# Kernel tuning notes

Measured on AMD Instinct MI355X. Metric: run time of the kernel, lower is better.

Reference implementation:

```python
import jax, jax.numpy as jnp
import numpy as np

B, T, N, FIN, FOUT, EDIM = 2, 32, 64, 64, 64, 16
EPS = 1e-5

def _xavier(key, fan_in, fan_out):
    limit = np.sqrt(6.0 / (fan_in + fan_out))
    return jax.random.uniform(key, (fan_in, fan_out), minval=-limit, maxval=limit, dtype=jnp.float32)

def setup_inputs() -> dict:
    key = jax.random.key(0)
    ks = jax.random.split(key, 8)
    x = jax.random.normal(ks[0], (B, T, N, FIN), dtype=jnp.float32)
    adj = jax.random.uniform(ks[1], (B, N, N), dtype=jnp.float32)
    # edge_net: Linear(1->EDIM), GELU, Linear(EDIM->FIN*FOUT); stored as (in,out)
    ew1 = _xavier(ks[2], 1, EDIM)
    eb1 = jnp.zeros((EDIM,), jnp.float32)
    ew2 = _xavier(ks[3], EDIM, FIN * FOUT)
    eb2 = jnp.zeros((FIN * FOUT,), jnp.float32)
    # node_lin: Linear(FIN->FOUT)
    nw = _xavier(ks[4], FIN, FOUT)
    nb = jnp.zeros((FOUT,), jnp.float32)
    # GraphNorm params (pre_norm -> num_features = FIN)
    gw = jnp.ones((FIN,), jnp.float32)
    gb = jnp.zeros((FIN,), jnp.float32)
    gms = jnp.ones((1,), jnp.float32)
    return {"x": x, "adj": adj, "ew1": ew1, "eb1": eb1, "ew2": ew2, "eb2": eb2,
            "nw": nw, "nb": nb, "gw": gw, "gb": gb, "gms": gms}

def reference(x, adj, ew1, eb1, ew2, eb2, nw, nb, gw, gb, gms):
    # GraphNorm over node axis (dim=-2), pre-norm
    mean = jnp.mean(x, axis=-2, keepdims=True)
    var = jnp.var(x, axis=-2, keepdims=True)  # unbiased=False
    xn = (x - mean * gms) / jnp.sqrt(var + EPS)
    xn = xn * gw + gb  # (B,T,N,FIN)
    # edge-conditioned weights: scalar adj -> (B,N,N,FIN,FOUT)
    ef = adj[..., None]  # (B,N,N,1)
    h = jax.nn.gelu(ef @ ew1 + eb1, approximate=False)  # (B,N,N,EDIM)
    edge_w = (h @ ew2 + eb2).reshape(adj.shape[0], N, N, FIN, FOUT)
    # agg[b,t,i,o] = sum_j sum_f xn[b,t,j,f] * edge_w[b,i,j,f,o]
    agg = jnp.einsum('btjf,bijfo->btio', xn, edge_w)
    y = xn @ nw + nb + agg
    y = jax.nn.gelu(y, approximate=False)  # torch nn.GELU default = exact erf
    return y
```

## Files before the change

kernel.cpp:

```cpp
#include <hip/hip_runtime.h>


#define LSTR 72
#define XSTR 68

typedef unsigned short u16;
typedef _Float16 f16;
typedef _Float16 f16x8 __attribute__((ext_vector_type(8)));
typedef _Float16 f16x4 __attribute__((ext_vector_type(4)));
typedef float f32x4 __attribute__((ext_vector_type(4)));

__device__ __forceinline__ float bf2f(u16 u) {
    union { unsigned int i; float f; } c; c.i = ((unsigned int)u) << 16; return c.f;
}
__device__ __forceinline__ u16 f2bf(float f) {
    union { float f; unsigned int i; } c; c.f = f;
    unsigned int r = c.i + 0x7FFFu + ((c.i >> 16) & 1u);
    return (u16)(r >> 16);
}
__device__ __forceinline__ float gelu_exact(float v) {
    return 0.5f * v * (1.0f + erff(v * 0.70710678118654752440f));
}
__device__ __forceinline__ float loadf(const void* p, int i, bool bf) {
    return bf ? bf2f(((const u16*)p)[i]) : ((const float*)p)[i];
}
__device__ __forceinline__ int detect_bf16(const void* xp) {
    const u16* u = (const u16*)xp;
    int sane = 0;
    #pragma unroll
    for (int k = 0; k < 64; ++k) {
        int e = (u[k * 2] >> 7) & 0xFF;
        sane += (e >= 100 && e <= 150);
    }
    return sane >= 40;
}

__global__ __launch_bounds__(256) void precomp(
    const void* __restrict__ adj, const void* __restrict__ ew1, const void* __restrict__ eb1,
    const void* __restrict__ ew2, const void* __restrict__ nw, const void* __restrict__ x,
    f16* __restrict__ H, f16* __restrict__ W2t, f16* __restrict__ NWt)
{
    const bool bf = detect_bf16(x) != 0;

    int idx = blockIdx.x * 256 + threadIdx.x;
    if (idx < 131072) {
        int b = idx >> 16, rem = idx & 65535, e = rem >> 12, ij = rem & 4095;
        float a = loadf(adj, (b << 12) + ij, bf);
        float v = a * loadf(ew1, e, bf) + loadf(eb1, e, bf);
        H[idx] = (f16)gelu_exact(v);
    } else if (idx < 196608) {
        int k = idx - 131072, e = k >> 12, of = k & 4095, o = of >> 6, f = of & 63;
        W2t[k] = (f16)loadf(ew2, (e << 12) + (f << 6) + o, bf);
    } else if (idx < 200704) {
        int k = idx - 196608, o = k >> 6, f = k & 63;
        NWt[k] = (f16)loadf(nw, (f << 6) + o, bf);
    }
}

__global__ __launch_bounds__(256) void fused_main(
    const void* __restrict__ x, const void* __restrict__ eb2, const void* __restrict__ nb,
    const void* __restrict__ gw, const void* __restrict__ gb, const void* __restrict__ gms,
    const f16* __restrict__ H, const f16* __restrict__ W2t, const f16* __restrict__ NWt,
    void* __restrict__ out)
{
    __shared__ float xraw[64 * XSTR];
    __shared__ f16 xn_lds[64 * LSTR];
    __shared__ f16 zt_lds[16 * 16 * LSTR];
    __shared__ float red1[256];
    __shared__ float red2[256];
    __shared__ float af[64], cf[64], Sv[64], t2o[64];

    const int tid  = threadIdx.x;
    const int blk  = blockIdx.x;
    const int bt   = blk >> 2;
    const int quar = blk & 3;
    const int b    = bt >> 5;
    const int lane = tid & 63;
    const int wave = tid >> 6;
    const int ln   = lane & 15;
    const int q    = lane >> 4;
    const int row  = tid >> 2;
    const int colb = (tid & 3) << 4;

    const bool bf = detect_bf16(x) != 0;

    {
        int base = (bt << 12) + (row << 6) + colb;
        if (bf) {
            const uint4* src = (const uint4*)((const u16*)x + base);
            uint4 v0 = src[0], v1 = src[1];
            const u16* p0 = (const u16*)&v0;
            const u16* p1 = (const u16*)&v1;
            #pragma unroll
            for (int k = 0; k < 8; ++k) {
                xraw[row * XSTR + colb + k]     = bf2f(p0[k]);
                xraw[row * XSTR + colb + 8 + k] = bf2f(p1[k]);
            }
        } else {
            const float4* src = (const float4*)((const float*)x + base);
            #pragma unroll
            for (int k = 0; k < 4; ++k) {
                float4 v = src[k];
                xraw[row * XSTR + colb + 4 * k]     = v.x;
                xraw[row * XSTR + colb + 4 * k + 1] = v.y;
                xraw[row * XSTR + colb + 4 * k + 2] = v.z;
                xraw[row * XSTR + colb + 4 * k + 3] = v.w;
            }
        }
    }
    __syncthreads();
    {
        int f = tid & 63, part = tid >> 6;
        float s1 = 0.f, s2 = 0.f;
        #pragma unroll
        for (int r = 0; r < 16; ++r) {
            float v = xraw[(part * 16 + r) * XSTR + f];
            s1 += v; s2 += v * v;
        }
        red1[part * 64 + f] = s1; red2[part * 64 + f] = s2;
    }
    __syncthreads();
    if (tid < 64) {
        float s1 = red1[tid] + red1[64 + tid] + red1[128 + tid] + red1[192 + tid];
        float s2 = red2[tid] + red2[64 + tid] + red2[128 + tid] + red2[192 + tid];
        float mean = s1 * 0.015625f;
        float var  = s2 * 0.015625f - mean * mean;
        float inv  = rsqrtf(var + 1e-5f);
        float gwf = loadf(gw, tid, bf), gbf = loadf(gb, tid, bf), g = loadf(gms, 0, bf);
        float a = inv * gwf;
        af[tid] = a;
        cf[tid] = gbf - mean * g * a;
        Sv[tid] = 64.f * (mean * (1.f - g) * a + gbf);
    }
    __syncthreads();
    {
        #pragma unroll
        for (int k = 0; k < 16; ++k) {
            int col = colb + k;
            xn_lds[row * LSTR + col] = (f16)(xraw[row * XSTR + col] * af[col] + cf[col]);
        }
    }
    {
        int o = tid & 63, part = tid >> 6;
        float s = 0.f;
        #pragma unroll
        for (int r = 0; r < 16; ++r) {
            int f = part * 16 + r;
            s += Sv[f] * loadf(eb2, (f << 6) + o, bf);
        }
        red1[part * 64 + o] = s;
    }
    __syncthreads();
    if (tid < 64)
        t2o[tid] = red1[tid] + red1[64 + tid] + red1[128 + tid] + red1[192 + tid]
                 + loadf(nb, tid, bf);

    f16x8 xa0 = *(const f16x8*)&xn_lds[(wave * 16 + ln) * LSTR + q * 8];
    f16x8 xa1 = *(const f16x8*)&xn_lds[(wave * 16 + ln) * LSTR + 32 + q * 8];

    #pragma unroll
    for (int e = 0; e < 16; ++e) {
        const f16* wrow = W2t + (((e << 6) + (quar << 4) + ln) << 6);
        f16x8 b0 = *(const f16x8*)(wrow + q * 8);
        f16x8 b1 = *(const f16x8*)(wrow + 32 + q * 8);
        f32x4 z = {0.f, 0.f, 0.f, 0.f};
        z = __builtin_amdgcn_mfma_f32_16x16x32_f16(xa0, b0, z, 0, 0, 0);
        z = __builtin_amdgcn_mfma_f32_16x16x32_f16(xa1, b1, z, 0, 0, 0);
        f16x4 p;
        #pragma unroll
        for (int r = 0; r < 4; ++r) p[r] = (f16)z[r];
        *(f16x4*)&zt_lds[((e << 4) + ln) * LSTR + wave * 16 + q * 4] = p;
    }
    __syncthreads();

    f32x4 acc0 = {0.f,0.f,0.f,0.f}, acc1 = {0.f,0.f,0.f,0.f};
    f32x4 acc2 = {0.f,0.f,0.f,0.f}, acc3 = {0.f,0.f,0.f,0.f};
    const f16* hbase = H + ((b * 16) << 12) + ((wave * 16 + ln) << 6) + q * 8;
    #pragma unroll
    for (int kk = 0; kk < 32; ++kk) {
        const int e = kk >> 1, jh = kk & 1;
        f16x8 ha = *(const f16x8*)(hbase + (e << 12) + jh * 32);
        f16x8 zb = *(const f16x8*)&zt_lds[((e << 4) + ln) * LSTR + jh * 32 + q * 8];
        switch (kk & 3) {
            case 0: acc0 = __builtin_amdgcn_mfma_f32_16x16x32_f16(ha, zb, acc0, 0, 0, 0); break;
            case 1: acc1 = __builtin_amdgcn_mfma_f32_16x16x32_f16(ha, zb, acc1, 0, 0, 0); break;
            case 2: acc2 = __builtin_amdgcn_mfma_f32_16x16x32_f16(ha, zb, acc2, 0, 0, 0); break;
            default: acc3 = __builtin_amdgcn_mfma_f32_16x16x32_f16(ha, zb, acc3, 0, 0, 0); break;
        }
    }
    {
        const f16* nrow = NWt + (((quar << 4) + ln) << 6);
        f16x8 b0 = *(const f16x8*)(nrow + q * 8);
        f16x8 b1 = *(const f16x8*)(nrow + 32 + q * 8);
        acc0 = __builtin_amdgcn_mfma_f32_16x16x32_f16(xa0, b0, acc0, 0, 0, 0);
        acc1 = __builtin_amdgcn_mfma_f32_16x16x32_f16(xa1, b1, acc1, 0, 0, 0);
    }
    {
        const int o = (quar << 4) + ln;
        const float add = t2o[o];
        if (bf) {
            u16* ob = (u16*)out + (bt << 12);
            #pragma unroll
            for (int r = 0; r < 4; ++r) {
                int i = wave * 16 + q * 4 + r;
                float v = acc0[r] + acc1[r] + acc2[r] + acc3[r] + add;
                ob[(i << 6) + o] = f2bf(gelu_exact(v));
            }
        } else {
            float* ob = (float*)out + (bt << 12);
            #pragma unroll
            for (int r = 0; r < 4; ++r) {
                int i = wave * 16 + q * 4 + r;
                float v = acc0[r] + acc1[r] + acc2[r] + acc3[r] + add;
                ob[(i << 6) + o] = gelu_exact(v);
            }
        }
    }
}

extern "C" void kernel_launch(void* const* d_in, const int* in_sizes, int n_in,
                              void* d_out, int out_size, void* d_ws, size_t ws_size,
                              hipStream_t stream) {
    const void* x   = d_in[0];
    const void* adj = d_in[1];
    const void* ew1 = d_in[2];
    const void* eb1 = d_in[3];
    const void* ew2 = d_in[4];
    const void* eb2 = d_in[5];
    const void* nw  = d_in[6];
    const void* nb  = d_in[7];
    const void* gw  = d_in[8];
    const void* gb  = d_in[9];
    const void* gms = d_in[10];

    f16* H   = (f16*)d_ws;
    f16* W2t = H + 131072;
    f16* NWt = W2t + 65536;

    precomp<<<784, 256, 0, stream>>>(adj, ew1, eb1, ew2, nw, x, H, W2t, NWt);
    fused_main<<<256, 256, 0, stream>>>(x, eb2, nb, gw, gb, gms, H, W2t, NWt, d_out);
}
```

Measured before the change: 91.07 us.

## Fuse precompute into main kernel with a software grid barrier

Folds the separate precompute launch into the main kernel. Each block computes its slice of the GELU edge features H, stages a transposed f16 copy of its ew2 and node-weight slice directly in shared memory, and waits on a global sense-reversal atomic barrier before reading H. The first half of the z-projection is computed before the barrier wait, so that work overlaps the other blocks' H writes, and the z buffer is split into two halves that share storage with xraw. This removes one kernel launch and the global W2t/NWt round trip. In exchange it depends on all 256 blocks being co-resident, and the spin loop bails out after a bounded count, which could let a block read incomplete H.

```diff
diff --git a/kernel.cpp b/kernel.cpp
--- a/kernel.cpp
+++ b/kernel.cpp
@@ -9,6 +9,9 @@
 typedef _Float16 f16x8 __attribute__((ext_vector_type(8)));
 typedef _Float16 f16x4 __attribute__((ext_vector_type(4)));
 typedef float f32x4 __attribute__((ext_vector_type(4)));
+
+__device__ unsigned g_bar_cnt = 0;
+__device__ unsigned g_bar_sense = 0;
 
 __device__ __forceinline__ float bf2f(u16 u) {
     union { unsigned int i; float f; } c; c.i = ((unsigned int)u) << 16; return c.f;
@@ -35,40 +38,25 @@
     return sane >= 40;
 }
 
-__global__ __launch_bounds__(256) void precomp(
-    const void* __restrict__ adj, const void* __restrict__ ew1, const void* __restrict__ eb1,
-    const void* __restrict__ ew2, const void* __restrict__ nw, const void* __restrict__ x,
-    f16* __restrict__ H, f16* __restrict__ W2t, f16* __restrict__ NWt)
-{
-    const bool bf = detect_bf16(x) != 0;
-
-    int idx = blockIdx.x * 256 + threadIdx.x;
-    if (idx < 131072) {
-        int b = idx >> 16, rem = idx & 65535, e = rem >> 12, ij = rem & 4095;
-        float a = loadf(adj, (b << 12) + ij, bf);
-        float v = a * loadf(ew1, e, bf) + loadf(eb1, e, bf);
-        H[idx] = (f16)gelu_exact(v);
-    } else if (idx < 196608) {
-        int k = idx - 131072, e = k >> 12, of = k & 4095, o = of >> 6, f = of & 63;
-        W2t[k] = (f16)loadf(ew2, (e << 12) + (f << 6) + o, bf);
-    } else if (idx < 200704) {
-        int k = idx - 196608, o = k >> 6, f = k & 63;
-        NWt[k] = (f16)loadf(nw, (f << 6) + o, bf);
-    }
-}
-
-__global__ __launch_bounds__(256) void fused_main(
-    const void* __restrict__ x, const void* __restrict__ eb2, const void* __restrict__ nb,
-    const void* __restrict__ gw, const void* __restrict__ gb, const void* __restrict__ gms,
-    const f16* __restrict__ H, const f16* __restrict__ W2t, const f16* __restrict__ NWt,
+__global__ __launch_bounds__(256) void fused_all(
+    const void* __restrict__ x, const void* __restrict__ adj,
+    const void* __restrict__ ew1, const void* __restrict__ eb1,
+    const void* __restrict__ ew2, const void* __restrict__ eb2,
+    const void* __restrict__ nw, const void* __restrict__ nb,
+    const void* __restrict__ gw, const void* __restrict__ gb,
+    const void* __restrict__ gms, f16* __restrict__ H,
     void* __restrict__ out)
 {
-    __shared__ float xraw[64 * XSTR];
+    __shared__ union {
+        float xraw[64 * XSTR];
+        f16 zt[8 * 16 * LSTR];
+    } uXZ;
     __shared__ f16 xn_lds[64 * LSTR];
-    __shared__ f16 zt_lds[16 * 16 * LSTR];
+    __shared__ f16 w2s[(16 * 16 + 16) * LSTR];
     __shared__ float red1[256];
     __shared__ float red2[256];
     __shared__ float af[64], cf[64], Sv[64], t2o[64];
+    __shared__ unsigned s_sense;
 
     const int tid  = threadIdx.x;
     const int blk  = blockIdx.x;
@@ -83,29 +71,85 @@
     const int colb = (tid & 3) << 4;
 
     const bool bf = detect_bf16(x) != 0;
-
+    float* xraw = uXZ.xraw;
+    f16*   zt   = uXZ.zt;
+
+    uint4 xb0, xb1; float4 xf[4];
     {
         int base = (bt << 12) + (row << 6) + colb;
         if (bf) {
             const uint4* src = (const uint4*)((const u16*)x + base);
-            uint4 v0 = src[0], v1 = src[1];
-            const u16* p0 = (const u16*)&v0;
-            const u16* p1 = (const u16*)&v1;
-            #pragma unroll
-            for (int k = 0; k < 8; ++k) {
-                xraw[row * XSTR + colb + k]     = bf2f(p0[k]);
-                xraw[row * XSTR + colb + 8 + k] = bf2f(p1[k]);
-            }
+            xb0 = src[0]; xb1 = src[1];
         } else {
             const float4* src = (const float4*)((const float*)x + base);
             #pragma unroll
-            for (int k = 0; k < 4; ++k) {
-                float4 v = src[k];
-                xraw[row * XSTR + colb + 4 * k]     = v.x;
-                xraw[row * XSTR + colb + 4 * k + 1] = v.y;
-                xraw[row * XSTR + colb + 4 * k + 2] = v.z;
-                xraw[row * XSTR + colb + 4 * k + 3] = v.w;
-            }
+            for (int k = 0; k < 4; ++k) xf[k] = src[k];
+        }
+    }
+
+    #pragma unroll
+    for (int it = 0; it < 2; ++it) {
+        int idx = (blk << 9) + (it << 8) + tid;
+        int hb = idx >> 16, rem = idx & 65535, e = rem >> 12, ij = rem & 4095;
+        float a = loadf(adj, (hb << 12) + ij, bf);
+        float v = a * loadf(ew1, e, bf) + loadf(eb1, e, bf);
+        H[idx] = (f16)gelu_exact(v);
+    }
+
+    if (bf) {
+        const u16* e2 = (const u16*)ew2;
+        int rv2 = tid >> 1, p2 = tid & 1, f = rv2 & 63;
+        #pragma unroll
+        for (int it = 0; it < 8; ++it) {
+            int rowi = rv2 + it * 128;
+            int e = rowi >> 6;
+            uint4 v = *(const uint4*)(e2 + (rowi << 6) + (quar << 4) + (p2 << 3));
+            const u16* pv = (const u16*)&v;
+            #pragma unroll
+            for (int k = 0; k < 8; ++k)
+                w2s[((e << 4) + (p2 << 3) + k) * LSTR + f] = (f16)bf2f(pv[k]);
+        }
+        const u16* nwb = (const u16*)nw;
+        int fr = tid >> 2, p = tid & 3;
+        uint2 v = *(const uint2*)(nwb + (fr << 6) + (quar << 4) + (p << 2));
+        const u16* pv = (const u16*)&v;
+        #pragma unroll
+        for (int k = 0; k < 4; ++k)
+            w2s[(256 + (p << 2) + k) * LSTR + fr] = (f16)bf2f(pv[k]);
+    } else {
+        const float* e2 = (const float*)ew2;
+        int rv = tid >> 2, p = tid & 3;
+        #pragma unroll
+        for (int eo = 0; eo < 16; ++eo) {
+            float4 v = *(const float4*)(e2 + (eo << 12) + (rv << 6) + (quar << 4) + (p << 2));
+            w2s[((eo << 4) + (p << 2) + 0) * LSTR + rv] = (f16)v.x;
+            w2s[((eo << 4) + (p << 2) + 1) * LSTR + rv] = (f16)v.y;
+            w2s[((eo << 4) + (p << 2) + 2) * LSTR + rv] = (f16)v.z;
+            w2s[((eo << 4) + (p << 2) + 3) * LSTR + rv] = (f16)v.w;
+        }
+        const float* nwf = (const float*)nw;
+        float4 v = *(const float4*)(nwf + (rv << 6) + (quar << 4) + (p << 2));
+        w2s[(256 + (p << 2) + 0) * LSTR + rv] = (f16)v.x;
+        w2s[(256 + (p << 2) + 1) * LSTR + rv] = (f16)v.y;
+        w2s[(256 + (p << 2) + 2) * LSTR + rv] = (f16)v.z;
+        w2s[(256 + (p << 2) + 3) * LSTR + rv] = (f16)v.w;
+    }
+
+    if (bf) {
+        const u16* p0 = (const u16*)&xb0;
+        const u16* p1 = (const u16*)&xb1;
+        #pragma unroll
+        for (int k = 0; k < 8; ++k) {
+            xraw[row * XSTR + colb + k]     = bf2f(p0[k]);
+            xraw[row * XSTR + colb + 8 + k] = bf2f(p1[k]);
+        }
+    } else {
+        #pragma unroll
+        for (int k = 0; k < 4; ++k) {
+            xraw[row * XSTR + colb + 4 * k]     = xf[k].x;
+            xraw[row * XSTR + colb + 4 * k + 1] = xf[k].y;
+            xraw[row * XSTR + colb + 4 * k + 2] = xf[k].z;
+            xraw[row * XSTR + colb + 4 * k + 3] = xf[k].w;
         }
     }
     __syncthreads();
@@ -131,6 +175,19 @@
         af[tid] = a;
         cf[tid] = gbf - mean * g * a;
         Sv[tid] = 64.f * (mean * (1.f - g) * a + gbf);
+    } else if (tid == 64) {
+        unsigned ms = __hip_atomic_load(&g_bar_sense, __ATOMIC_RELAXED,
+                                        __HIP_MEMORY_SCOPE_AGENT);
+        s_sense = ms;
+        __threadfence();
+        unsigned prev = __hip_atomic_fetch_add(&g_bar_cnt, 1u, __ATOMIC_ACQ_REL,
+                                               __HIP_MEMORY_SCOPE_AGENT);
+        if (prev == gridDim.x - 1) {
+            __hip_atomic_store(&g_bar_cnt, 0u, __ATOMIC_RELAXED,
+                               __HIP_MEMORY_SCOPE_AGENT);
+            __hip_atomic_fetch_add(&g_bar_sense, 1u, __ATOMIC_RELEASE,
+                                   __HIP_MEMORY_SCOPE_AGENT);
+        }
     }
     __syncthreads();
     {
@@ -158,38 +215,54 @@
     f16x8 xa0 = *(const f16x8*)&xn_lds[(wave * 16 + ln) * LSTR + q * 8];
     f16x8 xa1 = *(const f16x8*)&xn_lds[(wave * 16 + ln) * LSTR + 32 + q * 8];
 
-    #pragma unroll
-    for (int e = 0; e < 16; ++e) {
-        const f16* wrow = W2t + (((e << 6) + (quar << 4) + ln) << 6);
-        f16x8 b0 = *(const f16x8*)(wrow + q * 8);
-        f16x8 b1 = *(const f16x8*)(wrow + 32 + q * 8);
-        f32x4 z = {0.f, 0.f, 0.f, 0.f};
-        z = __builtin_amdgcn_mfma_f32_16x16x32_f16(xa0, b0, z, 0, 0, 0);
-        z = __builtin_amdgcn_mfma_f32_16x16x32_f16(xa1, b1, z, 0, 0, 0);
-        f16x4 p;
-        #pragma unroll
-        for (int r = 0; r < 4; ++r) p[r] = (f16)z[r];
-        *(f16x4*)&zt_lds[((e << 4) + ln) * LSTR + wave * 16 + q * 4] = p;
-    }
-    __syncthreads();
-
     f32x4 acc0 = {0.f,0.f,0.f,0.f}, acc1 = {0.f,0.f,0.f,0.f};
     f32x4 acc2 = {0.f,0.f,0.f,0.f}, acc3 = {0.f,0.f,0.f,0.f};
-    const f16* hbase = H + ((b * 16) << 12) + ((wave * 16 + ln) << 6) + q * 8;
+    const f16* hbase = H + (b << 16) + ((wave * 16 + ln) << 6) + q * 8;
+
     #pragma unroll
-    for (int kk = 0; kk < 32; ++kk) {
-        const int e = kk >> 1, jh = kk & 1;
-        f16x8 ha = *(const f16x8*)(hbase + (e << 12) + jh * 32);
-        f16x8 zb = *(const f16x8*)&zt_lds[((e << 4) + ln) * LSTR + jh * 32 + q * 8];
-        switch (kk & 3) {
-            case 0: acc0 = __builtin_amdgcn_mfma_f32_16x16x32_f16(ha, zb, acc0, 0, 0, 0); break;
-            case 1: acc1 = __builtin_amdgcn_mfma_f32_16x16x32_f16(ha, zb, acc1, 0, 0, 0); break;
-            case 2: acc2 = __builtin_amdgcn_mfma_f32_16x16x32_f16(ha, zb, acc2, 0, 0, 0); break;
-            default: acc3 = __builtin_amdgcn_mfma_f32_16x16x32_f16(ha, zb, acc3, 0, 0, 0); break;
-        }
-    }
-    {
-        const f16* nrow = NWt + (((quar << 4) + ln) << 6);
+    for (int r = 0; r < 2; ++r) {
+        #pragma unroll
+        for (int el = 0; el < 8; ++el) {
+            int e = r * 8 + el;
+            const f16* wrow = &w2s[((e << 4) + ln) * LSTR];
+            f16x8 b0 = *(const f16x8*)(wrow + q * 8);
+            f16x8 b1 = *(const f16x8*)(wrow + 32 + q * 8);
+            f32x4 z = {0.f, 0.f, 0.f, 0.f};
+            z = __builtin_amdgcn_mfma_f32_16x16x32_f16(xa0, b0, z, 0, 0, 0);
+            z = __builtin_amdgcn_mfma_f32_16x16x32_f16(xa1, b1, z, 0, 0, 0);
+            f16x4 p;
+            #pragma unroll
+            for (int rr = 0; rr < 4; ++rr) p[rr] = (f16)z[rr];
+            *(f16x4*)&zt[((el << 4) + ln) * LSTR + wave * 16 + q * 4] = p;
+        }
+        if (r == 0) {
+            if (tid == 0) {
+                unsigned ms = s_sense;
+                unsigned spins = 0;
+                while (__hip_atomic_load(&g_bar_sense, __ATOMIC_ACQUIRE,
+                                         __HIP_MEMORY_SCOPE_AGENT) == ms) {
+                    __builtin_amdgcn_s_sleep(2);
+                    if (++spins > (1u << 26)) break;
+                }
+            }
+        }
+        __syncthreads();
+        #pragma unroll
+        for (int kk = 0; kk < 16; ++kk) {
+            int el = kk >> 1, jh = kk & 1, e = r * 8 + el;
+            f16x8 ha = *(const f16x8*)(hbase + (e << 12) + jh * 32);
+            f16x8 zb = *(const f16x8*)&zt[((el << 4) + ln) * LSTR + jh * 32 + q * 8];
+            switch (kk & 3) {
+                case 0: acc0 = __builtin_amdgcn_mfma_f32_16x16x32_f16(ha, zb, acc0, 0, 0, 0); break;
+                case 1: acc1 = __builtin_amdgcn_mfma_f32_16x16x32_f16(ha, zb, acc1, 0, 0, 0); break;
+                case 2: acc2 = __builtin_amdgcn_mfma_f32_16x16x32_f16(ha, zb, acc2, 0, 0, 0); break;
+                default: acc3 = __builtin_amdgcn_mfma_f32_16x16x32_f16(ha, zb, acc3, 0, 0, 0); break;
+            }
+        }
+        if (r == 0) __syncthreads();
+    }
+    {
+        const f16* nrow = &w2s[(256 + ln) * LSTR];
         f16x8 b0 = *(const f16x8*)(nrow + q * 8);
         f16x8 b1 = *(const f16x8*)(nrow + 32 + q * 8);
         acc0 = __builtin_amdgcn_mfma_f32_16x16x32_f16(xa0, b0, acc0, 0, 0, 0);
@@ -201,17 +274,17 @@
         if (bf) {
             u16* ob = (u16*)out + (bt << 12);
             #pragma unroll
-            for (int r = 0; r < 4; ++r) {
-                int i = wave * 16 + q * 4 + r;
-                float v = acc0[r] + acc1[r] + acc2[r] + acc3[r] + add;
+            for (int rr = 0; rr < 4; ++rr) {
+                int i = wave * 16 + q * 4 + rr;
+                float v = acc0[rr] + acc1[rr] + acc2[rr] + acc3[rr] + add;
                 ob[(i << 6) + o] = f2bf(gelu_exact(v));
             }
         } else {
             float* ob = (float*)out + (bt << 12);
             #pragma unroll
-            for (int r = 0; r < 4; ++r) {
-                int i = wave * 16 + q * 4 + r;
-                float v = acc0[r] + acc1[r] + acc2[r] + acc3[r] + add;
+            for (int rr = 0; rr < 4; ++rr) {
+                int i = wave * 16 + q * 4 + rr;
+                float v = acc0[rr] + acc1[rr] + acc2[rr] + acc3[rr] + add;
                 ob[(i << 6) + o] = gelu_exact(v);
             }
         }
@@ -233,10 +306,8 @@
     const void* gb  = d_in[9];
     const void* gms = d_in[10];
 
-    f16* H   = (f16*)d_ws;
-    f16* W2t = H + 131072;
-    f16* NWt = W2t + 65536;
-
-    precomp<<<784, 256, 0, stream>>>(adj, ew1, eb1, ew2, nw, x, H, W2t, NWt);
-    fused_main<<<256, 256, 0, stream>>>(x, eb2, nb, gw, gb, gms, H, W2t, NWt, d_out);
-}
+    f16* H = (f16*)d_ws;
+
+    fused_all<<<256, 256, 0, stream>>>(x, adj, ew1, eb1, ew2, eb2, nw, nb,
+                                       gw, gb, gms, H, d_out);
+}
```

Measured after the change: 92.94 us. +2.1%, slower.

## Move GraphNorm normalization and bias terms into precompute kernel, dedupe per-quarter work

Applied to the files above, without the earlier changes.

Each of the 64 (b,t) slices now has one block in the precompute kernel. That block computes the node-axis mean and variance, the normalized fp16 activations, and the eb2/nb bias vector, and writes them to workspace. Before, each of the four output-quarter blocks in the main kernel repeated this work. The remaining precompute blocks each handle two elements per thread, and the bf16 flag is passed to the main kernel through workspace. The main kernel becomes a lean MFMA kernel that loads the normalized activations from global memory. The cost is an extra global round trip for those activations and a longer critical path in the first kernel.

```diff
diff --git a/kernel.cpp b/kernel.cpp
--- a/kernel.cpp
+++ b/kernel.cpp
@@ -35,54 +35,53 @@
     return sane >= 40;
 }
 
+
 __global__ __launch_bounds__(256) void precomp(
-    const void* __restrict__ adj, const void* __restrict__ ew1, const void* __restrict__ eb1,
-    const void* __restrict__ ew2, const void* __restrict__ nw, const void* __restrict__ x,
-    f16* __restrict__ H, f16* __restrict__ W2t, f16* __restrict__ NWt)
-{
-    const bool bf = detect_bf16(x) != 0;
-
-    int idx = blockIdx.x * 256 + threadIdx.x;
-    if (idx < 131072) {
-        int b = idx >> 16, rem = idx & 65535, e = rem >> 12, ij = rem & 4095;
-        float a = loadf(adj, (b << 12) + ij, bf);
-        float v = a * loadf(ew1, e, bf) + loadf(eb1, e, bf);
-        H[idx] = (f16)gelu_exact(v);
-    } else if (idx < 196608) {
-        int k = idx - 131072, e = k >> 12, of = k & 4095, o = of >> 6, f = of & 63;
-        W2t[k] = (f16)loadf(ew2, (e << 12) + (f << 6) + o, bf);
-    } else if (idx < 200704) {
-        int k = idx - 196608, o = k >> 6, f = k & 63;
-        NWt[k] = (f16)loadf(nw, (f << 6) + o, bf);
-    }
-}
-
-__global__ __launch_bounds__(256) void fused_main(
-    const void* __restrict__ x, const void* __restrict__ eb2, const void* __restrict__ nb,
-    const void* __restrict__ gw, const void* __restrict__ gb, const void* __restrict__ gms,
-    const f16* __restrict__ H, const f16* __restrict__ W2t, const f16* __restrict__ NWt,
-    void* __restrict__ out)
+    const void* __restrict__ x, const void* __restrict__ adj,
+    const void* __restrict__ ew1, const void* __restrict__ eb1,
+    const void* __restrict__ ew2, const void* __restrict__ eb2,
+    const void* __restrict__ nw, const void* __restrict__ nb,
+    const void* __restrict__ gw, const void* __restrict__ gb,
+    const void* __restrict__ gms, f16* __restrict__ ws)
 {
     __shared__ float xraw[64 * XSTR];
-    __shared__ f16 xn_lds[64 * LSTR];
-    __shared__ f16 zt_lds[16 * 16 * LSTR];
     __shared__ float red1[256];
     __shared__ float red2[256];
-    __shared__ float af[64], cf[64], Sv[64], t2o[64];
-
-    const int tid  = threadIdx.x;
-    const int blk  = blockIdx.x;
-    const int bt   = blk >> 2;
-    const int quar = blk & 3;
-    const int b    = bt >> 5;
-    const int lane = tid & 63;
-    const int wave = tid >> 6;
-    const int ln   = lane & 15;
-    const int q    = lane >> 4;
+    __shared__ float af[64], cf[64], Sv[64];
+
+    const int blk = blockIdx.x, tid = threadIdx.x;
+    const bool bf = detect_bf16(x) != 0;
+
+    if (blk >= 64) {
+        f16* H   = ws;
+        f16* W2t = ws + 131072;
+        f16* NWt = ws + 196608;
+        #pragma unroll
+        for (int it = 0; it < 2; ++it) {
+            int idx = ((blk - 64) << 9) + (it << 8) + tid;
+            if (idx < 131072) {
+                int b = idx >> 16, rem = idx & 65535, e = rem >> 12, ij = rem & 4095;
+                float a = loadf(adj, (b << 12) + ij, bf);
+                float v = a * loadf(ew1, e, bf) + loadf(eb1, e, bf);
+                H[idx] = (f16)gelu_exact(v);
+            } else if (idx < 196608) {
+                int k = idx - 131072, e = k >> 12, of = k & 4095, o = of >> 6, f = of & 63;
+                W2t[k] = (f16)loadf(ew2, (e << 12) + (f << 6) + o, bf);
+            } else if (idx < 200704) {
+                int k = idx - 196608, o = k >> 6, f = k & 63;
+                NWt[k] = (f16)loadf(nw, (f << 6) + o, bf);
+            }
+        }
+        return;
+    }
+
+    const int bt   = blk;
     const int row  = tid >> 2;
     const int colb = (tid & 3) << 4;
-
-    const bool bf = detect_bf16(x) != 0;
+    f16*   xn  = ws + 200704 + (bt << 12);
+    float* t2o = (float*)(ws + 462848) + (bt << 6);
+
+    if (blk == 0 && tid == 0) *(unsigned*)(ws + 471040) = bf ? 1u : 0u;
 
     {
         int base = (bt << 12) + (row << 6) + colb;
@@ -134,11 +133,14 @@
     }
     __syncthreads();
     {
+        f16 tmp[16];
         #pragma unroll
         for (int k = 0; k < 16; ++k) {
             int col = colb + k;
-            xn_lds[row * LSTR + col] = (f16)(xraw[row * XSTR + col] * af[col] + cf[col]);
-        }
+            tmp[k] = (f16)(xraw[row * XSTR + col] * af[col] + cf[col]);
+        }
+        *(f16x8*)&xn[(row << 6) + colb]     = *(f16x8*)&tmp[0];
+        *(f16x8*)&xn[(row << 6) + colb + 8] = *(f16x8*)&tmp[8];
     }
     {
         int o = tid & 63, part = tid >> 6;
@@ -154,9 +156,32 @@
     if (tid < 64)
         t2o[tid] = red1[tid] + red1[64 + tid] + red1[128 + tid] + red1[192 + tid]
                  + loadf(nb, tid, bf);
-
-    f16x8 xa0 = *(const f16x8*)&xn_lds[(wave * 16 + ln) * LSTR + q * 8];
-    f16x8 xa1 = *(const f16x8*)&xn_lds[(wave * 16 + ln) * LSTR + 32 + q * 8];
+}
+
+__global__ __launch_bounds__(256) void fused_main(
+    const f16* __restrict__ ws, void* __restrict__ out)
+{
+    __shared__ f16 zt[16 * 16 * LSTR];
+
+    const int tid  = threadIdx.x;
+    const int blk  = blockIdx.x;
+    const int bt   = blk >> 2;
+    const int quar = blk & 3;
+    const int b    = bt >> 5;
+    const int lane = tid & 63;
+    const int wave = tid >> 6;
+    const int ln   = lane & 15;
+    const int q    = lane >> 4;
+
+    const f16* H   = ws;
+    const f16* W2t = ws + 131072;
+    const f16* NWt = ws + 196608;
+    const f16* xn  = ws + 200704 + (bt << 12);
+    const float* t2o = (const float*)(ws + 462848) + (bt << 6);
+    const bool bf = *(const unsigned*)(ws + 471040) != 0;
+
+    f16x8 xa0 = *(const f16x8*)&xn[((wave * 16 + ln) << 6) + q * 8];
+    f16x8 xa1 = *(const f16x8*)&xn[((wave * 16 + ln) << 6) + 32 + q * 8];
 
     #pragma unroll
     for (int e = 0; e < 16; ++e) {
@@ -169,18 +194,18 @@
         f16x4 p;
         #pragma unroll
         for (int r = 0; r < 4; ++r) p[r] = (f16)z[r];
-        *(f16x4*)&zt_lds[((e << 4) + ln) * LSTR + wave * 16 + q * 4] = p;
+        *(f16x4*)&zt[((e << 4) + ln) * LSTR + wave * 16 + q * 4] = p;
     }
     __syncthreads();
 
     f32x4 acc0 = {0.f,0.f,0.f,0.f}, acc1 = {0.f,0.f,0.f,0.f};
     f32x4 acc2 = {0.f,0.f,0.f,0.f}, acc3 = {0.f,0.f,0.f,0.f};
-    const f16* hbase = H + ((b * 16) << 12) + ((wave * 16 + ln) << 6) + q * 8;
+    const f16* hbase = H + (b << 16) + ((wave * 16 + ln) << 6) + q * 8;
     #pragma unroll
     for (int kk = 0; kk < 32; ++kk) {
         const int e = kk >> 1, jh = kk & 1;
         f16x8 ha = *(const f16x8*)(hbase + (e << 12) + jh * 32);
-        f16x8 zb = *(const f16x8*)&zt_lds[((e << 4) + ln) * LSTR + jh * 32 + q * 8];
+        f16x8 zb = *(const f16x8*)&zt[((e << 4) + ln) * LSTR + jh * 32 + q * 8];
         switch (kk & 3) {
             case 0: acc0 = __builtin_amdgcn_mfma_f32_16x16x32_f16(ha, zb, acc0, 0, 0, 0); break;
             case 1: acc1 = __builtin_amdgcn_mfma_f32_16x16x32_f16(ha, zb, acc1, 0, 0, 0); break;
@@ -233,10 +258,9 @@
     const void* gb  = d_in[9];
     const void* gms = d_in[10];
 
-    f16* H   = (f16*)d_ws;
-    f16* W2t = H + 131072;
-    f16* NWt = W2t + 65536;
-
-    precomp<<<784, 256, 0, stream>>>(adj, ew1, eb1, ew2, nw, x, H, W2t, NWt);
-    fused_main<<<256, 256, 0, stream>>>(x, eb2, nb, gw, gb, gms, H, W2t, NWt, d_out);
-}
+    f16* ws = (f16*)d_ws;
+
+    precomp<<<512, 256, 0, stream>>>(x, adj, ew1, eb1, ew2, eb2, nw, nb,
+                                     gw, gb, gms, ws);
+    fused_main<<<256, 256, 0, stream>>>(ws, d_out);
+}
```

After: 87.57 us. 1.04x faster.
